# Kernel tuning notes

Measured on AMD Instinct MI355X. Metric: run time of the kernel, lower is better.

Reference implementation:

```python
import math
import jax, jax.numpy as jnp
import numpy as np

B, T, H = 2, 2048, 1024
NH, WINDOW = 16, 256
HD = H // NH


def setup_inputs() -> dict:
    key = jax.random.key(0)
    ks = jax.random.split(key, 4)
    x = jax.random.normal(ks[0], (B, T, H), dtype=jnp.float32)
    # init scales match nn.Linear default fan-in uniform roughly; exact init irrelevant for correctness
    W_qkv = jax.random.normal(ks[1], (H, 3 * H), dtype=jnp.float32) * (1.0 / math.sqrt(H))
    b_qkv = jnp.zeros((3 * H,), dtype=jnp.float32)
    W_out = jax.random.normal(ks[2], (H, H), dtype=jnp.float32) * (1.0 / math.sqrt(H))
    b_out = jnp.zeros((H,), dtype=jnp.float32)
    return {"x": x, "W_qkv": W_qkv, "b_qkv": b_qkv, "W_out": W_out, "b_out": b_out}


def reference(x, W_qkv, b_qkv, W_out, b_out):
    b, t, h = x.shape
    qkv = x @ W_qkv + b_qkv                      # [B, T, 3H]
    qkv = qkv.reshape(b, t, 3, NH, HD)           # (three nh hd) split order
    qkv = jnp.transpose(qkv, (2, 0, 3, 1, 4))    # [3, B, nh, T, hd]
    q, k, v = qkv[0], qkv[1], qkv[2]
    scores = jnp.einsum('bnid,bnjd->bnij', q, k) / math.sqrt(HD)  # [B, nh, T, T]
    idx = jnp.arange(t)
    diff = idx[:, None] - idx[None, :]           # i - j
    mask = (diff < 0) | (diff >= WINDOW)         # causal + window band
    scores = jnp.where(mask[None, None], -jnp.inf, scores)
    attn = jax.nn.softmax(scores, axis=-1)
    out = jnp.einsum('bnij,bnjd->bnid', attn, v)  # [B, nh, T, hd]
    out = jnp.transpose(out, (0, 2, 1, 3)).reshape(b, t, h)
    return out @ W_out + b_out
```

## Files before the change

### kernel.cpp

```cpp
#include <hip/hip_runtime.h>

typedef unsigned short u16;
typedef __attribute__((ext_vector_type(8))) __bf16 bf16x8;
typedef __attribute__((ext_vector_type(4))) float f32x4;
typedef __attribute__((ext_vector_type(8))) u16 u16x8;

#define MFMA(a, b, c) __builtin_amdgcn_mfma_f32_16x16x32_bf16((a), (b), (c), 0, 0, 0)

#define TT 2048
#define NHEAD 16
#define HDIM 64

__device__ __forceinline__ u16 f2bf(float f) {
  union { float f; unsigned u; } v; v.f = f;
  unsigned r = (v.u + 0x7fffu + ((v.u >> 16) & 1u)) >> 16;
  return (u16)r;
}

__device__ __forceinline__ void gll16(const u16* g, u16* l) {
  __builtin_amdgcn_global_load_lds(
      (__attribute__((address_space(1))) void*)g,
      (__attribute__((address_space(3))) void*)l, 16, 0, 0);
}

__global__ __launch_bounds__(256) void cvt_bf16_k(const float* __restrict__ in,
                                                  u16* __restrict__ out) {
  int i = blockIdx.x * 256 + threadIdx.x;
  float4 a = ((const float4*)in)[2 * i];
  float4 b = ((const float4*)in)[2 * i + 1];
  u16x8 r;
  r[0] = f2bf(a.x); r[1] = f2bf(a.y); r[2] = f2bf(a.z); r[3] = f2bf(a.w);
  r[4] = f2bf(b.x); r[5] = f2bf(b.y); r[6] = f2bf(b.z); r[7] = f2bf(b.w);
  ((u16x8*)out)[i] = r;
}

__global__ __launch_bounds__(256) void transpose_cvt_k(const float* __restrict__ in,
                                                       u16* __restrict__ out,
                                                       int R, int C) {
  __shared__ float tile[32][33];
  int tx = threadIdx.x & 31, ty = threadIdx.x >> 5;
  int r0 = blockIdx.y * 32, c0 = blockIdx.x * 32;
#pragma unroll
  for (int i = 0; i < 4; ++i)
    tile[ty + i * 8][tx] = in[(size_t)(r0 + ty + i * 8) * C + c0 + tx];
  __syncthreads();
#pragma unroll
  for (int i = 0; i < 4; ++i)
    out[(size_t)(c0 + ty + i * 8) * R + r0 + tx] = f2bf(tile[tx][ty + i * 8]);
}

__device__ __forceinline__ void gemm_core(const u16* __restrict__ A,
                                          const u16* __restrict__ Bt,
                                          int m0, int n0,
                                          u16* As, u16* Bs, f32x4 acc[4][4]) {
  const int tid = threadIdx.x;
  const int w = tid >> 6, lane = tid & 63;
  const int wr = w >> 1, wc = w & 1;
  const int lr = lane & 15, lk = (lane >> 4) << 3;
  const int srow = w << 5;
  const u16* ga = A + (size_t)(m0 + srow + (lane >> 2)) * 1024 + ((lane & 3) << 3);
  const u16* gb = Bt + (size_t)(n0 + srow + (lane >> 2)) * 1024 + ((lane & 3) << 3);
  u16* la = As + srow * 32;
  u16* lb = Bs + srow * 32;
  for (int k0 = 0; k0 < 1024; k0 += 32) {
#pragma unroll
    for (int i = 0; i < 2; ++i) {
      gll16(ga + i * 16384 + k0, la + i * 512);
      gll16(gb + i * 16384 + k0, lb + i * 512);
    }
    __syncthreads();
    bf16x8 af[4], bfr[4];
#pragma unroll
    for (int m = 0; m < 4; ++m)
      af[m] = *(const bf16x8*)(As + ((wr << 6) + m * 16 + lr) * 32 + lk);
#pragma unroll
    for (int n = 0; n < 4; ++n)
      bfr[n] = *(const bf16x8*)(Bs + ((wc << 6) + n * 16 + lr) * 32 + lk);
#pragma unroll
    for (int m = 0; m < 4; ++m)
#pragma unroll
      for (int n = 0; n < 4; ++n)
        acc[m][n] = MFMA(af[m], bfr[n], acc[m][n]);
    __syncthreads();
  }
}

__global__ __launch_bounds__(256) void gemm_qkv_k(const u16* __restrict__ A,
                                                  const u16* __restrict__ Bt,
                                                  const float* __restrict__ bias,
                                                  u16* __restrict__ qo,
                                                  u16* __restrict__ ko,
                                                  u16* __restrict__ vto) {
  __shared__ __align__(16) u16 As[128 * 32];
  __shared__ __align__(16) u16 Bs[128 * 32];
  f32x4 acc[4][4] = {};
  const int m0 = blockIdx.y << 7, n0 = blockIdx.x << 7;
  gemm_core(A, Bt, m0, n0, As, Bs, acc);
  const int tid = threadIdx.x, w = tid >> 6, lane = tid & 63;
  const int wr = w >> 1, wc = w & 1, lr = lane & 15, lg = lane >> 4;
  const int gcb = n0 + (wc << 6);
  const int three = gcb >> 10;
  const int nh = (gcb & 1023) >> 6;
#pragma unroll
  for (int n = 0; n < 4; ++n) {
    const int hd = n * 16 + lr;
    const float bv = bias[gcb + hd];
#pragma unroll
    for (int m = 0; m < 4; ++m) {
#pragma unroll
      for (int r = 0; r < 4; ++r) {
        const int grow = m0 + (wr << 6) + m * 16 + (lg << 2) + r;
        const int bb = grow >> 11, t = grow & 2047;
        const float val = acc[m][n][r] + bv;
        const int head = (bb << 4) + nh;
        if (three == 0)
          qo[((size_t)head * TT + t) * HDIM + hd] = f2bf(val * 0.125f);
        else if (three == 1)
          ko[((size_t)head * TT + t) * HDIM + hd] = f2bf(val);
        else
          vto[((size_t)head * HDIM + hd) * TT + t] = f2bf(val);
      }
    }
  }
}

__global__ __launch_bounds__(256) void attn_win_k(const u16* __restrict__ Q,
                                                  const u16* __restrict__ K,
                                                  const u16* __restrict__ Vt,
                                                  u16* __restrict__ O) {
  __shared__ __align__(16) u16 Pl[4][16][72];
  const int tid = threadIdx.x, w = tid >> 6, lane = tid & 63;
  const int head = blockIdx.y;
  const int t0w = blockIdx.x * 64 + w * 16;
  const u16* Qh = Q + (size_t)head * TT * HDIM;
  const u16* Kh = K + (size_t)head * TT * HDIM;
  const u16* Vh = Vt + (size_t)head * HDIM * TT;
  const int lr = lane & 15, lg = lane >> 4;

  bf16x8 qa0 = *(const bf16x8*)(Qh + (size_t)(t0w + lr) * HDIM + lg * 8);
  bf16x8 qa1 = *(const bf16x8*)(Qh + (size_t)(t0w + lr) * HDIM + 32 + lg * 8);

  union { u16x8 u; bf16x8 b; } uo;
#pragma unroll
  for (int i = 0; i < 8; ++i) uo.u[i] = 0x3F80;
  const bf16x8 ones = uo.b;

  f32x4 o0 = {}, o1 = {}, o2 = {}, o3 = {}, osum = {};
  float m[4];
#pragma unroll
  for (int r = 0; r < 4; ++r) m[r] = -1e30f;

  const int jstart = (t0w > 255) ? ((t0w - 255) & ~63) : 0;
  const int jlast = t0w + 15;
  for (int j0 = jstart; j0 <= jlast; j0 += 64) {
    f32x4 s[4];
#pragma unroll
    for (int n = 0; n < 4; ++n) {
      const u16* kp = Kh + (size_t)(j0 + n * 16 + lr) * HDIM + lg * 8;
      f32x4 z = {};
      z = MFMA(qa0, *(const bf16x8*)kp, z);
      z = MFMA(qa1, *(const bf16x8*)(kp + 32), z);
      s[n] = z;
    }
    const int row0 = t0w + (lg << 2);
    float tm[4];
#pragma unroll
    for (int r = 0; r < 4; ++r) {
      const int i = row0 + r;
#pragma unroll
      for (int n = 0; n < 4; ++n) {
        const int j = j0 + n * 16 + lr;
        const bool valid = (j <= i) && (i - j < 256);
        s[n][r] = valid ? s[n][r] : -1e30f;
      }
      tm[r] = fmaxf(fmaxf(s[0][r], s[1][r]), fmaxf(s[2][r], s[3][r]));
    }
#pragma unroll
    for (int d = 1; d < 16; d <<= 1)
#pragma unroll
      for (int r = 0; r < 4; ++r) tm[r] = fmaxf(tm[r], __shfl_xor(tm[r], d));
    float sc[4];
#pragma unroll
    for (int r = 0; r < 4; ++r) {
      const float mn = fmaxf(m[r], tm[r]);
      sc[r] = __expf(m[r] - mn);
      m[r] = mn;
    }
#pragma unroll
    for (int n = 0; n < 4; ++n)
#pragma unroll
      for (int r = 0; r < 4; ++r)
        s[n][r] = __expf(s[n][r] - m[r]);
#pragma unroll
    for (int r = 0; r < 4; ++r) {
      o0[r] *= sc[r]; o1[r] *= sc[r]; o2[r] *= sc[r]; o3[r] *= sc[r];
      osum[r] *= sc[r];
    }
#pragma unroll
    for (int n = 0; n < 4; ++n)
#pragma unroll
      for (int r = 0; r < 4; ++r)
        Pl[w][(lg << 2) + r][n * 16 + lr] = f2bf(s[n][r]);
    asm volatile("s_waitcnt lgkmcnt(0)" ::: "memory");
    bf16x8 pa0 = *(const bf16x8*)&Pl[w][lr][lg * 8];
    bf16x8 pa1 = *(const bf16x8*)&Pl[w][lr][32 + lg * 8];
    const u16* vp = Vh + (size_t)lr * TT + j0 + lg * 8;
    o0 = MFMA(pa0, *(const bf16x8*)(vp), o0);
    o0 = MFMA(pa1, *(const bf16x8*)(vp + 32), o0);
    o1 = MFMA(pa0, *(const bf16x8*)(vp + 16 * TT), o1);
    o1 = MFMA(pa1, *(const bf16x8*)(vp + 16 * TT + 32), o1);
    o2 = MFMA(pa0, *(const bf16x8*)(vp + 32 * TT), o2);
    o2 = MFMA(pa1, *(const bf16x8*)(vp + 32 * TT + 32), o2);
    o3 = MFMA(pa0, *(const bf16x8*)(vp + 48 * TT), o3);
    o3 = MFMA(pa1, *(const bf16x8*)(vp + 48 * TT + 32), o3);
    osum = MFMA(pa0, ones, osum);
    osum = MFMA(pa1, ones, osum);
  }
  const int bb = head >> 4, nh = head & 15;
#pragma unroll
  for (int r = 0; r < 4; ++r) {
    const float inv = 1.0f / osum[r];
    const int i = t0w + (lg << 2) + r;
    u16* op = O + ((size_t)bb * TT + i) * 1024 + nh * 64 + lr;
    op[0]  = f2bf(o0[r] * inv);
    op[16] = f2bf(o1[r] * inv);
    op[32] = f2bf(o2[r] * inv);
    op[48] = f2bf(o3[r] * inv);
  }
}

__global__ __launch_bounds__(256) void gemm_out_k(const u16* __restrict__ A,
                                                  const u16* __restrict__ Bt,
                                                  const float* __restrict__ bias,
                                                  float* __restrict__ out) {
  __shared__ __align__(16) u16 As[64 * 32];
  __shared__ __align__(16) u16 Bs[128 * 32];
  f32x4 acc[2][4] = {};
  const int m0 = blockIdx.y << 6, n0 = blockIdx.x << 7;
  const int tid = threadIdx.x, w = tid >> 6, lane = tid & 63;
  const int wr = w >> 1, wc = w & 1, lr = lane & 15, lg = lane >> 4;
  const int lk = lg << 3;
  const u16* ga = A + (size_t)(m0 + (w << 4) + (lane >> 2)) * 1024 + ((lane & 3) << 3);
  const u16* gb = Bt + (size_t)(n0 + (w << 5) + (lane >> 2)) * 1024 + ((lane & 3) << 3);
  u16* la = As + (w << 4) * 32;
  u16* lb = Bs + (w << 5) * 32;
  for (int k0 = 0; k0 < 1024; k0 += 32) {
    gll16(ga + k0, la);
    gll16(gb + k0, lb);
    gll16(gb + 16384 + k0, lb + 512);
    __syncthreads();
    bf16x8 af[2], bfr[4];
#pragma unroll
    for (int m = 0; m < 2; ++m)
      af[m] = *(const bf16x8*)(As + ((wr << 5) + m * 16 + lr) * 32 + lk);
#pragma unroll
    for (int n = 0; n < 4; ++n)
      bfr[n] = *(const bf16x8*)(Bs + ((wc << 6) + n * 16 + lr) * 32 + lk);
#pragma unroll
    for (int m = 0; m < 2; ++m)
#pragma unroll
      for (int n = 0; n < 4; ++n)
        acc[m][n] = MFMA(af[m], bfr[n], acc[m][n]);
    __syncthreads();
  }
#pragma unroll
  for (int n = 0; n < 4; ++n) {
    const int gc = n0 + (wc << 6) + n * 16 + lr;
    const float bv = bias[gc];
#pragma unroll
    for (int m = 0; m < 2; ++m)
#pragma unroll
      for (int r = 0; r < 4; ++r) {
        const int grow = m0 + (wr << 5) + m * 16 + (lg << 2) + r;
        out[(size_t)grow * 1024 + gc] = acc[m][n][r] + bv;
      }
  }
}

extern "C" void kernel_launch(void* const* d_in, const int* in_sizes, int n_in,
                              void* d_out, int out_size, void* d_ws, size_t ws_size,
                              hipStream_t stream) {
  (void)in_sizes; (void)n_in; (void)out_size; (void)ws_size;
  const float* x    = (const float*)d_in[0];
  const float* Wqkv = (const float*)d_in[1];
  const float* bqkv = (const float*)d_in[2];
  const float* Wout = (const float*)d_in[3];
  const float* bout = (const float*)d_in[4];
  float* out = (float*)d_out;

  u16* ws    = (u16*)d_ws;
  u16* xb    = ws;
  u16* wqkvT = xb + 4194304;
  u16* woutT = wqkvT + 3145728;
  u16* qb    = woutT + 1048576;
  u16* kb    = qb + 4194304;
  u16* vtb   = kb + 4194304;
  u16* aob   = vtb + 4194304;

  cvt_bf16_k<<<2048, 256, 0, stream>>>(x, xb);
  transpose_cvt_k<<<dim3(3072 / 32, 1024 / 32), 256, 0, stream>>>(Wqkv, wqkvT, 1024, 3072);
  transpose_cvt_k<<<dim3(1024 / 32, 1024 / 32), 256, 0, stream>>>(Wout, woutT, 1024, 1024);
  gemm_qkv_k<<<dim3(24, 32), 256, 0, stream>>>(xb, wqkvT, bqkv, qb, kb, vtb);
  attn_win_k<<<dim3(32, 32), 256, 0, stream>>>(qb, kb, vtb, aob);
  gemm_out_k<<<dim3(8, 64), 256, 0, stream>>>(aob, woutT, bout, out);
}
```

Before: 188.3 us.

## Double-buffer LDS in GEMM core and reuse it for output projection

The shared GEMM core loop now uses two LDS buffers, so the next K-slice is prefetched with global_load_lds while MFMAs run on the current slice, with one barrier per iteration instead of two. The output projection kernel drops its own 64x128 loop and calls the shared 128x128 core, which halves its grid. This is meant to hide global load latency and improve reuse per tile. In exchange it doubles LDS per block, which may reduce occupancy, and the out-projection grid becomes 256 blocks, which may underfill the GPU.

Result: no change. 190.6 us (+1.2%).

```diff
diff --git a/kernel.cpp b/kernel.cpp
--- a/kernel.cpp
+++ b/kernel.cpp
@@ -62,27 +62,39 @@
   const u16* gb = Bt + (size_t)(n0 + srow + (lane >> 2)) * 1024 + ((lane & 3) << 3);
   u16* la = As + srow * 32;
   u16* lb = Bs + srow * 32;
+
+#define STAGE_G(buf, k0)                         \
+  {                                              \
+    gll16(ga + (k0), la + (buf) * 4096);         \
+    gll16(ga + 16384 + (k0), la + (buf) * 4096 + 512); \
+    gll16(gb + (k0), lb + (buf) * 4096);         \
+    gll16(gb + 16384 + (k0), lb + (buf) * 4096 + 512); \
+  }
+
+  STAGE_G(0, 0)
+  __syncthreads();
+  int cur = 0;
   for (int k0 = 0; k0 < 1024; k0 += 32) {
-#pragma unroll
-    for (int i = 0; i < 2; ++i) {
-      gll16(ga + i * 16384 + k0, la + i * 512);
-      gll16(gb + i * 16384 + k0, lb + i * 512);
-    }
-    __syncthreads();
+    const int nxt = k0 + 32;
+    if (nxt < 1024) STAGE_G(cur ^ 1, nxt)
+    const u16* as = As + cur * 4096;
+    const u16* bs = Bs + cur * 4096;
     bf16x8 af[4], bfr[4];
 #pragma unroll
     for (int m = 0; m < 4; ++m)
-      af[m] = *(const bf16x8*)(As + ((wr << 6) + m * 16 + lr) * 32 + lk);
+      af[m] = *(const bf16x8*)(as + ((wr << 6) + m * 16 + lr) * 32 + lk);
 #pragma unroll
     for (int n = 0; n < 4; ++n)
-      bfr[n] = *(const bf16x8*)(Bs + ((wc << 6) + n * 16 + lr) * 32 + lk);
+      bfr[n] = *(const bf16x8*)(bs + ((wc << 6) + n * 16 + lr) * 32 + lk);
 #pragma unroll
     for (int m = 0; m < 4; ++m)
 #pragma unroll
       for (int n = 0; n < 4; ++n)
         acc[m][n] = MFMA(af[m], bfr[n], acc[m][n]);
     __syncthreads();
-  }
+    cur ^= 1;
+  }
+#undef STAGE_G
 }
 
 __global__ __launch_bounds__(256) void gemm_qkv_k(const u16* __restrict__ A,
@@ -91,8 +103,8 @@
                                                   u16* __restrict__ qo,
                                                   u16* __restrict__ ko,
                                                   u16* __restrict__ vto) {
-  __shared__ __align__(16) u16 As[128 * 32];
-  __shared__ __align__(16) u16 Bs[128 * 32];
+  __shared__ __align__(16) u16 As[2 * 128 * 32];
+  __shared__ __align__(16) u16 Bs[2 * 128 * 32];
   f32x4 acc[4][4] = {};
   const int m0 = blockIdx.y << 7, n0 = blockIdx.x << 7;
   gemm_core(A, Bt, m0, n0, As, Bs, acc);
@@ -233,45 +245,22 @@
                                                   const u16* __restrict__ Bt,
                                                   const float* __restrict__ bias,
                                                   float* __restrict__ out) {
-  __shared__ __align__(16) u16 As[64 * 32];
-  __shared__ __align__(16) u16 Bs[128 * 32];
-  f32x4 acc[2][4] = {};
-  const int m0 = blockIdx.y << 6, n0 = blockIdx.x << 7;
+  __shared__ __align__(16) u16 As[2 * 128 * 32];
+  __shared__ __align__(16) u16 Bs[2 * 128 * 32];
+  f32x4 acc[4][4] = {};
+  const int m0 = blockIdx.y << 7, n0 = blockIdx.x << 7;
+  gemm_core(A, Bt, m0, n0, As, Bs, acc);
   const int tid = threadIdx.x, w = tid >> 6, lane = tid & 63;
   const int wr = w >> 1, wc = w & 1, lr = lane & 15, lg = lane >> 4;
-  const int lk = lg << 3;
-  const u16* ga = A + (size_t)(m0 + (w << 4) + (lane >> 2)) * 1024 + ((lane & 3) << 3);
-  const u16* gb = Bt + (size_t)(n0 + (w << 5) + (lane >> 2)) * 1024 + ((lane & 3) << 3);
-  u16* la = As + (w << 4) * 32;
-  u16* lb = Bs + (w << 5) * 32;
-  for (int k0 = 0; k0 < 1024; k0 += 32) {
-    gll16(ga + k0, la);
-    gll16(gb + k0, lb);
-    gll16(gb + 16384 + k0, lb + 512);
-    __syncthreads();
-    bf16x8 af[2], bfr[4];
-#pragma unroll
-    for (int m = 0; m < 2; ++m)
-      af[m] = *(const bf16x8*)(As + ((wr << 5) + m * 16 + lr) * 32 + lk);
-#pragma unroll
-    for (int n = 0; n < 4; ++n)
-      bfr[n] = *(const bf16x8*)(Bs + ((wc << 6) + n * 16 + lr) * 32 + lk);
-#pragma unroll
-    for (int m = 0; m < 2; ++m)
-#pragma unroll
-      for (int n = 0; n < 4; ++n)
-        acc[m][n] = MFMA(af[m], bfr[n], acc[m][n]);
-    __syncthreads();
-  }
 #pragma unroll
   for (int n = 0; n < 4; ++n) {
     const int gc = n0 + (wc << 6) + n * 16 + lr;
     const float bv = bias[gc];
 #pragma unroll
-    for (int m = 0; m < 2; ++m)
+    for (int m = 0; m < 4; ++m)
 #pragma unroll
       for (int r = 0; r < 4; ++r) {
-        const int grow = m0 + (wr << 5) + m * 16 + (lg << 2) + r;
+        const int grow = m0 + (wr << 6) + m * 16 + (lg << 2) + r;
         out[(size_t)grow * 1024 + gc] = acc[m][n][r] + bv;
       }
   }
@@ -302,5 +291,5 @@
   transpose_cvt_k<<<dim3(1024 / 32, 1024 / 32), 256, 0, stream>>>(Wout, woutT, 1024, 1024);
   gemm_qkv_k<<<dim3(24, 32), 256, 0, stream>>>(xb, wqkvT, bqkv, qb, kb, vtb);
   attn_win_k<<<dim3(32, 32), 256, 0, stream>>>(qb, kb, vtb, aob);
-  gemm_out_k<<<dim3(8, 64), 256, 0, stream>>>(aob, woutT, bout, out);
-}
+  gemm_out_k<<<dim3(8, 32), 256, 0, stream>>>(aob, woutT, bout, out);
+}
```
